# Optimization experiments

Measured on AMD Instinct MI355X. Metric: run time of the kernel, lower is better.

Reference implementation:

```python
import jax, jax.numpy as jnp
import numpy as np

H, HD = 8, 64  # num_heads, head_dim
EPS = 1e-6

def rmsnorm(x, scale):
    return x * jax.lax.rsqrt(jnp.mean(x * x, axis=-1, keepdims=True) + EPS) * scale

def lecun(key, shape):
    fan_in = shape[0]
    return jax.random.normal(key, shape, dtype=jnp.float32) * (fan_in ** -0.5)

def setup_inputs() -> dict:
    key = jax.random.key(0)
    ks = jax.random.split(key, 12)
    B, S, D = 2, 512, 512
    hidden = H * HD            # 512
    ffn = 4 * D                # 2048
    return {
        "inputs": jax.random.normal(ks[0], (B, S, D), dtype=jnp.float32),
        "mask": jnp.zeros((B, S), dtype=jnp.float32),
        "carry": jnp.zeros((B, H, HD, HD), dtype=jnp.float32),
        "ln1": jnp.ones((D,), dtype=jnp.float32),
        "Wq": lecun(ks[1], (D, hidden)),
        "Wk": lecun(ks[2], (D, hidden)),
        "Wv": lecun(ks[3], (D, hidden)),
        "attn_ln": jnp.ones((hidden,), dtype=jnp.float32),
        "Wo": lecun(ks[4], (hidden, D)),
        "bo": jnp.zeros((D,), dtype=jnp.float32),
        "ln2": jnp.ones((D,), dtype=jnp.float32),
        "Wg": lecun(ks[5], (D, ffn)),
        "Wu": lecun(ks[6], (D, ffn)),
        "Wd": lecun(ks[7], (ffn, D)),
    }

def reference(inputs, mask, carry, ln1, Wq, Wk, Wv, attn_ln, Wo, bo, ln2, Wg, Wu, Wd):
    B, S, D = inputs.shape
    skip = inputs
    x = rmsnorm(inputs, ln1)
    # projections + relu feature map
    q = jax.nn.relu((x @ Wq).reshape(B, S, H, HD))
    k = jax.nn.relu((x @ Wk).reshape(B, S, H, HD))
    v = (x @ Wv).reshape(B, S, H, HD)
    # matrix-valued state update: Bmat_t = v_t k_t^T  [B,S,H,HD,HD]
    Bmat = v[..., :, None] * k[..., None, :]
    # decay: identity, zeroed where mask==1 (episode reset)
    m = mask[:, :, None, None, None]
    A = jnp.broadcast_to(jnp.eye(HD, dtype=x.dtype), Bmat.shape) * (1.0 - m)

    def binop(lhs, rhs):
        a_i, b_i = lhs
        a_j, b_j = rhs
        return jnp.matmul(a_i, a_j), jnp.matmul(b_i, a_j) + b_j

    cum_decay, hidden_states = jax.lax.associative_scan(binop, (A, Bmat), axis=1)
    # fold in incoming carry
    states = jnp.matmul(carry[:, None], cum_decay) + hidden_states  # [B,S,H,HD,HD]
    attn = jnp.matmul(states, q[..., None]).squeeze(-1).reshape(B, S, H * HD)
    attn = rmsnorm(attn, attn_ln)
    y = attn @ Wo + bo
    final_carry = states[:, -1]
    # residual + SwiGLU FFN
    x = y + skip
    skip2 = x
    x = rmsnorm(x, ln2)
    x = (jax.nn.silu(x @ Wg) * (x @ Wu)) @ Wd
    return (final_carry, x + skip2)
```

## Files before the change

### kernel.cpp

```cpp
#include <hip/hip_runtime.h>
#include <math.h>

typedef __bf16 bf16x8 __attribute__((ext_vector_type(8)));
typedef float  f32x4  __attribute__((ext_vector_type(4)));

constexpr int B_=2, S_=512, D_=512, H_=8, HD_=64, FFN_=2048, NC_=8;
constexpr float EPS_=1e-6f;

__device__ __forceinline__ __bf16 f2bf(float f){
    union{float f;unsigned u;}x; x.f=f;
    unsigned r=(x.u+0x7fffu+((x.u>>16)&1u))>>16;
    union{unsigned short s;__bf16 b;}y; y.s=(unsigned short)r; return y.b;
}
__device__ __forceinline__ float bf2f(unsigned short s){
    union{unsigned u;float f;}x; x.u=((unsigned)s)<<16; return x.f;
}
__device__ __forceinline__ void bf8_f32(uint4 p, float* o){
    unsigned w[4]={p.x,p.y,p.z,p.w};
#pragma unroll
    for(int i=0;i<4;i++){ o[2*i]=bf2f((unsigned short)(w[i]&0xffffu)); o[2*i+1]=bf2f((unsigned short)(w[i]>>16)); }
}
__device__ __forceinline__ f32x4 MF(bf16x8 a, bf16x8 b, f32x4 c){
    return __builtin_amdgcn_mfma_f32_16x16x32_bf16(a,b,c,0,0,0);
}
#define GLOAD16(g,l) __builtin_amdgcn_global_load_lds((__attribute__((address_space(1))) const void*)(g),(__attribute__((address_space(3))) void*)(l),16,0,0)

__device__ __forceinline__ void rowsq_atomic(float* accb, int row0, int lane, float p[4]){
#pragma unroll
    for(int r=0;r<4;r++){
        float v = p[r];
        v += __shfl_xor(v, 1, 64);
        v += __shfl_xor(v, 2, 64);
        v += __shfl_xor(v, 4, 64);
        v += __shfl_xor(v, 8, 64);
        if((lane&15)==0) atomicAdd(accb + row0 + r, v);
    }
}

__global__ __launch_bounds__(256) void prep_k(const float* __restrict__ Wg,
    const float* __restrict__ Wu, const float* __restrict__ Wd,
    const float* __restrict__ Wq, const float* __restrict__ Wk,
    const float* __restrict__ Wv, const float* __restrict__ Wo,
    __bf16* __restrict__ WT, const float* __restrict__ inputs,
    float* __restrict__ rs1, float* __restrict__ rs2acc, float* __restrict__ rs3acc){
    __shared__ __bf16 s[64][72];
    int t = blockIdx.x, tid = threadIdx.x;
    if(t >= 1024){
        int row = (t-1024)*4 + (tid>>6), lane = tid&63;
        const float4* p = (const float4*)(inputs + (size_t)row*D_) + lane*2;
        float4 a=p[0], b=p[1];
        float ss = a.x*a.x+a.y*a.y+a.z*a.z+a.w*a.w + b.x*b.x+b.y*b.y+b.z*b.z+b.w*b.w;
        for(int off=32; off>0; off>>=1) ss += __shfl_down(ss, off, 64);
        if(lane==0) rs1[row] = rsqrtf(ss/(float)D_ + EPS_);
        float4 z = {0.f,0.f,0.f,0.f};
        if(t==1024) ((float4*)rs2acc)[tid] = z;
        if(t==1025) ((float4*)rs3acc)[tid] = z;
        return;
    }
    const float* src; __bf16* dst; int K,N,lt;
    if      (t<256){ src=Wg; dst=WT;          K=512;  N=2048; lt=t; }
    else if (t<512){ src=Wu; dst=WT+1048576;  K=512;  N=2048; lt=t-256; }
    else if (t<768){ src=Wd; dst=WT+2097152;  K=2048; N=512;  lt=t-512; }
    else if (t<832){ src=Wq; dst=WT+3145728;  K=512;  N=512;  lt=t-768; }
    else if (t<896){ src=Wk; dst=WT+3407872;  K=512;  N=512;  lt=t-832; }
    else if (t<960){ src=Wv; dst=WT+3670016;  K=512;  N=512;  lt=t-896; }
    else           { src=Wo; dst=WT+3932160;  K=512;  N=512;  lt=t-960; }
    int nt64 = N>>6, tk = lt/nt64, tn = lt%nt64;
    {
        int jk = tid>>2, jn0 = (tid&3)*16;
        const float* p = src + (size_t)(tk*64+jk)*N + tn*64 + jn0;
        float4 a0=((const float4*)p)[0], a1=((const float4*)p)[1],
               a2=((const float4*)p)[2], a3=((const float4*)p)[3];
        bf16x8 w0, w1;
        w0[0]=f2bf(a0.x); w0[1]=f2bf(a0.y); w0[2]=f2bf(a0.z); w0[3]=f2bf(a0.w);
        w0[4]=f2bf(a1.x); w0[5]=f2bf(a1.y); w0[6]=f2bf(a1.z); w0[7]=f2bf(a1.w);
        w1[0]=f2bf(a2.x); w1[1]=f2bf(a2.y); w1[2]=f2bf(a2.z); w1[3]=f2bf(a2.w);
        w1[4]=f2bf(a3.x); w1[5]=f2bf(a3.y); w1[6]=f2bf(a3.z); w1[7]=f2bf(a3.w);
        *(bf16x8*)&s[jk][jn0] = w0; *(bf16x8*)&s[jk][jn0+8] = w1;
    }
    __syncthreads();
    {
        int jn = tid&63, jkq = (tid>>6)*16;
        bf16x8 w0, w1;
#pragma unroll
        for(int j=0;j<8;j++){ w0[j]=s[jkq+j][jn]; w1[j]=s[jkq+8+j][jn]; }
        __bf16* q = dst + (size_t)(tn*64+jn)*K + tk*64 + jkq;
        *(bf16x8*)q = w0; *(bf16x8*)(q+8) = w1;
    }
}

__device__ __forceinline__ void stageB1(const __bf16* __restrict__ Bt, int n0, int K, int kk,
                                        __bf16* sB0, __bf16* sB1, int wave, int lane){
    int row = (wave<<4) + (lane>>2), kq = (lane&3)<<3;
    const __bf16* g = Bt + (size_t)(n0+row)*K + kk + kq;
    GLOAD16(g,      sB0 + (wave<<9));
    GLOAD16(g + 32, sB1 + (wave<<9));
}
struct ARf { float4 a0,a1,a2,a3, g0,g1,g2,g3; };
__device__ __forceinline__ ARf loadA_f32(const float* __restrict__ A, const float* __restrict__ g,
                                         int m0, int K, int kk, int tid){
    int row = tid>>2, kq = (tid&3)<<4;
    const float4* p = (const float4*)(A + (size_t)(m0+row)*K + kk + kq);
    const float4* gp = (const float4*)(g + kk + kq);
    ARf o;
    o.a0=p[0]; o.a1=p[1]; o.a2=p[2]; o.a3=p[3];
    o.g0=gp[0]; o.g1=gp[1]; o.g2=gp[2]; o.g3=gp[3];
    return o;
}
__device__ __forceinline__ void writeA_f32(const ARf& o, float r, __bf16* sA0, __bf16* sA1, int tid){
    int row = tid>>2, kq = (tid&3)<<4;
    bf16x8 w0, w1;
    w0[0]=f2bf(o.a0.x*r*o.g0.x); w0[1]=f2bf(o.a0.y*r*o.g0.y);
    w0[2]=f2bf(o.a0.z*r*o.g0.z); w0[3]=f2bf(o.a0.w*r*o.g0.w);
    w0[4]=f2bf(o.a1.x*r*o.g1.x); w0[5]=f2bf(o.a1.y*r*o.g1.y);
    w0[6]=f2bf(o.a1.z*r*o.g1.z); w0[7]=f2bf(o.a1.w*r*o.g1.w);
    w1[0]=f2bf(o.a2.x*r*o.g2.x); w1[1]=f2bf(o.a2.y*r*o.g2.y);
    w1[2]=f2bf(o.a2.z*r*o.g2.z); w1[3]=f2bf(o.a2.w*r*o.g2.w);
    w1[4]=f2bf(o.a3.x*r*o.g3.x); w1[5]=f2bf(o.a3.y*r*o.g3.y);
    w1[6]=f2bf(o.a3.z*r*o.g3.z); w1[7]=f2bf(o.a3.w*r*o.g3.w);
    __bf16* d = (kq<32) ? (sA0 + row*32 + kq) : (sA1 + row*32 + kq-32);
    *(bf16x8*)d = w0; *(bf16x8*)(d+8) = w1;
}
struct ARb { uint4 p0,p1; float4 g0,g1,g2,g3; };
__device__ __forceinline__ ARb loadA_bf16(const __bf16* __restrict__ A, const float* __restrict__ g,
                                          int m0, int K, int kk, int tid){
    int row = tid>>2, kq = (tid&3)<<4;
    const __bf16* p = A + (size_t)(m0+row)*K + kk + kq;
    const float4* gp = (const float4*)(g + kk + kq);
    ARb o;
    o.p0 = *(const uint4*)p; o.p1 = *(const uint4*)(p+8);
    o.g0=gp[0]; o.g1=gp[1]; o.g2=gp[2]; o.g3=gp[3];
    return o;
}
__device__ __forceinline__ void writeA_bf16(const ARb& o, float r, __bf16* sA0, __bf16* sA1, int tid){
    int row = tid>>2, kq = (tid&3)<<4;
    float v[16]; bf8_f32(o.p0, v); bf8_f32(o.p1, v+8);
    float gf[16] = {o.g0.x,o.g0.y,o.g0.z,o.g0.w, o.g1.x,o.g1.y,o.g1.z,o.g1.w,
                    o.g2.x,o.g2.y,o.g2.z,o.g2.w, o.g3.x,o.g3.y,o.g3.z,o.g3.w};
    bf16x8 w0, w1;
#pragma unroll
    for(int j=0;j<8;j++){ w0[j]=f2bf(v[j]*r*gf[j]); w1[j]=f2bf(v[8+j]*r*gf[8+j]); }
    __bf16* d = (kq<32) ? (sA0 + row*32 + kq) : (sA1 + row*32 + kq-32);
    *(bf16x8*)d = w0; *(bf16x8*)(d+8) = w1;
}
__device__ __forceinline__ void mfma_tile(const __bf16* sA0, const __bf16* sA1,
        const __bf16* sB0, const __bf16* sB1, int wave, int lane, f32x4 acc[4]){
    int ar = (((wave<<4)+(lane&15))<<5) + ((lane>>4)<<3);
    bf16x8 a0 = *(const bf16x8*)(sA0+ar);
    bf16x8 a1 = *(const bf16x8*)(sA1+ar);
#pragma unroll
    for(int nt=0;nt<4;nt++){
        int br = (((nt<<4)+(lane&15))<<5) + ((lane>>4)<<3);
        acc[nt] = MF(a0, *(const bf16x8*)(sB0+br), acc[nt]);
        acc[nt] = MF(a1, *(const bf16x8*)(sB1+br), acc[nt]);
    }
}

__global__ __launch_bounds__(256) void gemm_qkv_k(const float* __restrict__ in,
        const float* __restrict__ rs1, const float* __restrict__ ln1,
        const __bf16* __restrict__ Bt, __bf16* __restrict__ Qb,
        __bf16* __restrict__ Kb, __bf16* __restrict__ Vb){
    __shared__ __bf16 sA0[2][2048], sA1[2][2048], sB0[2][2048], sB1[2][2048];
    int tid=threadIdx.x, wave=tid>>6, lane=tid&63;
    int n0 = blockIdx.x*64, m0 = blockIdx.y*64;
    float r = rs1[m0+(tid>>2)];
    f32x4 acc[4] = {};
    {
        ARf a = loadA_f32(in, ln1, m0, 512, 0, tid);
        stageB1(Bt, n0, 512, 0, sB0[0], sB1[0], wave, lane);
        writeA_f32(a, r, sA0[0], sA1[0], tid);
        __syncthreads();
    }
    int cur = 0;
#pragma unroll
    for(int it=0; it<8; ++it){
        int nxt = cur^1;
        ARf a;
        if(it<7){
            a = loadA_f32(in, ln1, m0, 512, (it+1)*64, tid);
            stageB1(Bt, n0, 512, (it+1)*64, sB0[nxt], sB1[nxt], wave, lane);
        }
        mfma_tile(sA0[cur],sA1[cur],sB0[cur],sB1[cur],wave,lane,acc);
        if(it<7) writeA_f32(a, r, sA0[nxt], sA1[nxt], tid);
        __syncthreads();
        cur = nxt;
    }
    int seg = n0>>9, nc = n0&511;
    __bf16* Out = seg==0 ? Qb : (seg==1 ? Kb : Vb);
    bool rl = seg<2;
    __bf16* tile = &sA0[0][0];
    int r0 = (wave<<4) + ((lane>>4)<<2);
#pragma unroll
    for(int nt=0;nt<4;nt++){
        int col = nt*16 + (lane&15);
#pragma unroll
        for(int rr=0;rr<4;rr++){
            float v = acc[nt][rr]; if(rl) v = fmaxf(v,0.f);
            tile[(r0+rr)*64 + col] = f2bf(v);
        }
    }
    __syncthreads();
#pragma unroll
    for(int p=0;p<2;p++){
        int row = (tid>>3) + p*32, c0 = (tid&7)*8;
        *(uint4*)(Out + (size_t)(m0+row)*512 + nc + c0) = *(const uint4*)&tile[row*64 + c0];
    }
}

__global__ __launch_bounds__(256) void scanA_k(const __bf16* __restrict__ Kb,
        const __bf16* __restrict__ Vb, const float* __restrict__ mask,
        __bf16* __restrict__ MS, float* __restrict__ Pws){
    int bid = blockIdx.x;
    int c = bid&7, h = (bid>>3)&7, b = bid>>6;
    __shared__ __bf16 sKT[4096], sVT[4096];
    __shared__ float scv[64], ssp[64];
    int tid = threadIdx.x, wave = tid>>6, lane = tid&63;
    const __bf16* Kg = Kb + (size_t)(b*512 + c*64)*512 + h*64;
    const __bf16* Vg = Vb + (size_t)(b*512 + c*64)*512 + h*64;
    if(tid<64) scv[tid] = 1.f - mask[b*512 + c*64 + tid];
    __syncthreads();
    if(tid==0){
        float sp = 1.f;
        for(int t=63;t>=0;--t){ ssp[t]=sp; sp*=scv[t]; }
        Pws[bid] = sp;
    }
    __syncthreads();
#pragma unroll
    for(int p=0;p<2;p++){
        int t = (tid>>3) + p*32, i0 = (tid&7)*8;
        uint4 kr = *(const uint4*)(Kg + (size_t)t*512 + i0);
        uint4 vr = *(const uint4*)(Vg + (size_t)t*512 + i0);
        const __bf16* kp = (const __bf16*)&kr;
        const unsigned short* vp = (const unsigned short*)&vr;
        float sp = ssp[t];
        __bf16* kh = (t<32) ? sKT : sKT+2048;
        __bf16* vh = (t<32) ? sVT : sVT+2048;
#pragma unroll
        for(int j=0;j<8;j++){
            kh[(i0+j)*32 + (t&31)] = kp[j];
            vh[(i0+j)*32 + (t&31)] = f2bf(bf2f(vp[j])*sp);
        }
    }
    __syncthreads();
    f32x4 am[4] = {};
    mfma_tile(sVT, sVT+2048, sKT, sKT+2048, wave, lane, am);
    __bf16* Mo = MS + (size_t)bid*4096;
    int r0 = (wave<<4) + ((lane>>4)<<2);
#pragma unroll
    for(int nt=0;nt<4;nt++){
        int j = nt*16 + (lane&15);
#pragma unroll
        for(int r=0;r<4;r++) Mo[(size_t)(r0+r)*64 + j] = f2bf(am[nt][r]);
    }
}

__global__ __launch_bounds__(256) void scanC_k(const __bf16* __restrict__ Qb,
        const __bf16* __restrict__ Kb, const __bf16* __restrict__ Vb,
        const float* __restrict__ mask, const __bf16* __restrict__ MS,
        const float* __restrict__ carry, const float* __restrict__ Pws,
        float* __restrict__ carry_out, __bf16* __restrict__ attn,
        float* __restrict__ rs2acc){
    int bid = blockIdx.x;
    int c = bid&7, h = (bid>>3)&7, b = bid>>6;
    int bh = b*H_ + h;
    __shared__ __bf16 sQ[4096], sK[4096], sS[4096], sVT[4096], sW[4096];
    __shared__ float Wtab[64][64];
    __shared__ float scv[64], pp[64];
    int tid = threadIdx.x, wave = tid>>6, lane = tid&63;
    const __bf16* Qg = Qb + (size_t)(b*512 + c*64)*512 + h*64;
    const __bf16* Kg = Kb + (size_t)(b*512 + c*64)*512 + h*64;
    const __bf16* Vg = Vb + (size_t)(b*512 + c*64)*512 + h*64;

    stageB1(Qg, 0, 512, 0, sQ, sQ+2048, wave, lane);
    stageB1(Kg, 0, 512, 0, sK, sK+2048, wave, lane);
    if(tid<64) scv[tid] = 1.f - mask[b*512 + c*64 + tid];
#pragma unroll
    for(int p=0;p<2;p++){
        int u = (tid>>3) + p*32, i0 = (tid&7)*8;
        uint4 vr = *(const uint4*)(Vg + (size_t)u*512 + i0);
        const __bf16* vp = (const __bf16*)&vr;
        __bf16* vh = (u<32) ? sVT : sVT+2048;
#pragma unroll
        for(int j=0;j<8;j++) vh[(i0+j)*32 + (u&31)] = vp[j];
    }
    {
        int i = tid>>2, j0 = (tid&3)*16;
        float s[16];
        const float4* c4 = (const float4*)(carry + (size_t)bh*4096 + i*64 + j0);
        float4 s4[4] = {c4[0],c4[1],c4[2],c4[3]};
        float* sp = (float*)s4;
#pragma unroll
        for(int j=0;j<16;j++) s[j]=sp[j];
        for(int cc=0; cc<c; ++cc){
            float P = Pws[bh*8+cc];
            const __bf16* mp = MS + ((size_t)bh*8+cc)*4096 + i*64 + j0;
            float mv[16]; bf8_f32(*(const uint4*)mp, mv); bf8_f32(*(const uint4*)(mp+8), mv+8);
#pragma unroll
            for(int j=0;j<16;j++) s[j] = s[j]*P + mv[j];
        }
        bf16x8 w0, w1;
#pragma unroll
        for(int j=0;j<8;j++){ w0[j]=f2bf(s[j]); w1[j]=f2bf(s[8+j]); }
        __bf16* d = (j0<32) ? (sS + i*32 + j0) : (sS+2048 + i*32 + j0-32);
        *(bf16x8*)d = w0; *(bf16x8*)(d+8) = w1;
        if(c==7){
            float P = Pws[bh*8+7];
            const __bf16* mp = MS + ((size_t)bh*8+7)*4096 + i*64 + j0;
            float mv[16]; bf8_f32(*(const uint4*)mp, mv); bf8_f32(*(const uint4*)(mp+8), mv+8);
            float4 o4[4];
            float* ov = (float*)o4;
#pragma unroll
            for(int j=0;j<16;j++) ov[j] = s[j]*P + mv[j];
            float4* co = (float4*)(carry_out + (size_t)bh*4096 + i*64 + j0);
            co[0]=o4[0]; co[1]=o4[1]; co[2]=o4[2]; co[3]=o4[3];
        }
    }
    __syncthreads();
    if(tid<64){
        int u = tid; float w = 1.f;
        for(int t=0;t<64;t++){
            if(t>u) w *= scv[t];
            Wtab[u][t] = (t<u) ? 0.f : w;
        }
    }
    if(tid==64){
        float p=1.f;
        for(int t=0;t<64;t++){ p*=scv[t]; pp[t]=p; }
    }
    f32x4 sc[4] = {};
    mfma_tile(sK, sK+2048, sQ, sQ+2048, wave, lane, sc);
    __syncthreads();
    {
        int u0 = (wave<<4) + ((lane>>4)<<2);
#pragma unroll
        for(int nt=0;nt<4;nt++){
            int t = nt*16 + (lane&15);
#pragma unroll
            for(int r=0;r<4;r++){
                int u = u0 + r;
                float v = sc[nt][r] * Wtab[u][t];
                ((u<32)? sW : sW+2048)[t*32 + (u&31)] = f2bf(v);
            }
        }
    }
    __syncthreads();
    f32x4 aI[4] = {}, aX[4] = {};
    mfma_tile(sW, sW+2048, sVT, sVT+2048, wave, lane, aI);
    mfma_tile(sQ, sQ+2048, sS, sS+2048, wave, lane, aX);
    int t0 = (wave<<4) + ((lane>>4)<<2);
    float attv[4][4];
    float psum[4] = {0.f,0.f,0.f,0.f};
#pragma unroll
    for(int nt=0;nt<4;nt++){
#pragma unroll
        for(int r=0;r<4;r++){
            int t = t0 + r;
            float o = aI[nt][r] + aX[nt][r]*pp[t];
            attv[nt][r] = o;
            psum[r] += o*o;
        }
    }
    rowsq_atomic(rs2acc, b*512 + c*64 + t0, lane, psum);
    __syncthreads();
    __bf16* tile = sW;
#pragma unroll
    for(int nt=0;nt<4;nt++){
        int i = nt*16 + (lane&15);
#pragma unroll
        for(int r=0;r<4;r++) tile[(t0+r)*64 + i] = f2bf(attv[nt][r]);
    }
    __syncthreads();
#pragma unroll
    for(int p=0;p<2;p++){
        int row = (tid>>3) + p*32, c0 = (tid&7)*8;
        *(uint4*)(attn + (size_t)(b*512 + c*64 + row)*512 + h*64 + c0) =
            *(const uint4*)&tile[row*64 + c0];
    }
}

__global__ __launch_bounds__(256) void gemm_wo_k(const __bf16* __restrict__ attn,
        const float* __restrict__ rs2acc, const float* __restrict__ aln,
        const __bf16* __restrict__ Bt, const float* __restrict__ bo,
        const float* __restrict__ skip, float* __restrict__ outx,
        __bf16* __restrict__ X1, float* __restrict__ rs3acc){
    __shared__ __bf16 sA0[2][2048], sA1[2][2048], sB0[2][2048], sB1[2][2048];
    int tid=threadIdx.x, wave=tid>>6, lane=tid&63;
    int n0 = blockIdx.x*64, m0 = blockIdx.y*64;
    float r = rsqrtf(rs2acc[m0+(tid>>2)]*(1.f/(float)D_) + EPS_);
    f32x4 acc[4] = {};
    {
        ARb a = loadA_bf16(attn, aln, m0, 512, 0, tid);
        stageB1(Bt, n0, 512, 0, sB0[0], sB1[0], wave, lane);
        writeA_bf16(a, r, sA0[0], sA1[0], tid);
        __syncthreads();
    }
    int cur = 0;
#pragma unroll
    for(int it=0; it<8; ++it){
        int nxt = cur^1;
        ARb a;
        if(it<7){
            a = loadA_bf16(attn, aln, m0, 512, (it+1)*64, tid);
            stageB1(Bt, n0, 512, (it+1)*64, sB0[nxt], sB1[nxt], wave, lane);
        }
        mfma_tile(sA0[cur],sA1[cur],sB0[cur],sB1[cur],wave,lane,acc);
        if(it<7) writeA_bf16(a, r, sA0[nxt], sA1[nxt], tid);
        __syncthreads();
        cur = nxt;
    }
    int r0 = (wave<<4) + ((lane>>4)<<2);
    float psum[4] = {0.f,0.f,0.f,0.f};
    __bf16* tile = &sA0[0][0];
#pragma unroll
    for(int nt=0;nt<4;nt++){
        int col = n0 + nt*16 + (lane&15);
#pragma unroll
        for(int rr=0;rr<4;rr++){
            int row = m0+r0+rr;
            float v = acc[nt][rr] + bo[col] + skip[(size_t)row*512+col];
            outx[(size_t)row*512+col] = v;
            tile[(r0+rr)*64 + nt*16 + (lane&15)] = f2bf(v);
            psum[rr] += v*v;
        }
    }
    rowsq_atomic(rs3acc, m0+r0, lane, psum);
    __syncthreads();
#pragma unroll
    for(int p=0;p<2;p++){
        int row = (tid>>3) + p*32, c0 = (tid&7)*8;
        *(uint4*)(X1 + (size_t)(m0+row)*512 + n0 + c0) = *(const uint4*)&tile[row*64 + c0];
    }
}

__global__ __launch_bounds__(256) void gemm_dual_k(const __bf16* __restrict__ X1,
        const float* __restrict__ rs3acc, const float* __restrict__ ln2,
        const __bf16* __restrict__ Gt, const __bf16* __restrict__ Ut,
        __bf16* __restrict__ Hb){
    __shared__ __bf16 sA0[2][2048], sA1[2][2048];
    __shared__ __bf16 sG0[2][2048], sG1[2][2048], sU0[2][2048], sU1[2][2048];
    int tid=threadIdx.x, wave=tid>>6, lane=tid&63;
    int n0 = blockIdx.x*64, m0 = blockIdx.y*64;
    float r = rsqrtf(rs3acc[m0+(tid>>2)]*(1.f/(float)D_) + EPS_);
    f32x4 ag[4] = {}, au[4] = {};
    {
        ARb a = loadA_bf16(X1, ln2, m0, 512, 0, tid);
        stageB1(Gt, n0, 512, 0, sG0[0], sG1[0], wave, lane);
        stageB1(Ut, n0, 512, 0, sU0[0], sU1[0], wave, lane);
        writeA_bf16(a, r, sA0[0], sA1[0], tid);
        __syncthreads();
    }
    int cur = 0;
#pragma unroll
    for(int it=0; it<8; ++it){
        int nxt = cur^1;
        ARb a;
        if(it<7){
            a = loadA_bf16(X1, ln2, m0, 512, (it+1)*64, tid);
            stageB1(Gt, n0, 512, (it+1)*64, sG0[nxt], sG1[nxt], wave, lane);
            stageB1(Ut, n0, 512, (it+1)*64, sU0[nxt], sU1[nxt], wave, lane);
        }
        {
            int ar = (((wave<<4)+(lane&15))<<5) + ((lane>>4)<<3);
            bf16x8 a0 = *(const bf16x8*)(sA0[cur]+ar);
            bf16x8 a1 = *(const bf16x8*)(sA1[cur]+ar);
#pragma unroll
            for(int nt=0;nt<4;nt++){
                int br = (((nt<<4)+(lane&15))<<5) + ((lane>>4)<<3);
                ag[nt] = MF(a0, *(const bf16x8*)(sG0[cur]+br), ag[nt]);
                ag[nt] = MF(a1, *(const bf16x8*)(sG1[cur]+br), ag[nt]);
                au[nt] = MF(a0, *(const bf16x8*)(sU0[cur]+br), au[nt]);
                au[nt] = MF(a1, *(const bf16x8*)(sU1[cur]+br), au[nt]);
            }
        }
        if(it<7) writeA_bf16(a, r, sA0[nxt], sA1[nxt], tid);
        __syncthreads();
        cur = nxt;
    }
    int r0 = (wave<<4) + ((lane>>4)<<2);
    __bf16* tile = &sA0[0][0];
#pragma unroll
    for(int nt=0;nt<4;nt++){
        int col = nt*16 + (lane&15);
#pragma unroll
        for(int rr=0;rr<4;rr++){
            float gv = ag[nt][rr], uv = au[nt][rr];
            float hv = (gv / (1.f + __expf(-gv))) * uv;
            tile[(r0+rr)*64 + col] = f2bf(hv);
        }
    }
    __syncthreads();
#pragma unroll
    for(int p=0;p<2;p++){
        int row = (tid>>3) + p*32, c0 = (tid&7)*8;
        *(uint4*)(Hb + (size_t)(m0+row)*FFN_ + n0 + c0) = *(const uint4*)&tile[row*64 + c0];
    }
}

__global__ __launch_bounds__(256) void gemm_wd_k(const __bf16* __restrict__ Hb,
        const __bf16* __restrict__ Bt, float* __restrict__ outx){
    __shared__ __bf16 sA0[2][2048], sA1[2][2048], sB0[2][2048], sB1[2][2048];
    int tid=threadIdx.x, wave=tid>>6, lane=tid&63;
    int n0 = blockIdx.x*64, m0 = blockIdx.y*64, ks = blockIdx.z*512;
    f32x4 acc[4] = {};
    int row = (wave<<4) + (lane>>2), kq = (lane&3)<<3;
    {
        stageB1(Bt, n0, FFN_, ks, sB0[0], sB1[0], wave, lane);
        const __bf16* g = Hb + (size_t)(m0+row)*FFN_ + ks + kq;
        GLOAD16(g,      sA0[0] + (wave<<9));
        GLOAD16(g + 32, sA1[0] + (wave<<9));
        __syncthreads();
    }
    int cur = 0;
#pragma unroll
    for(int it=0; it<8; ++it){
        int nxt = cur^1;
        if(it<7){
            int kk = ks + (it+1)*64;
            stageB1(Bt, n0, FFN_, kk, sB0[nxt], sB1[nxt], wave, lane);
            const __bf16* g = Hb + (size_t)(m0+row)*FFN_ + kk + kq;
            GLOAD16(g,      sA0[nxt] + (wave<<9));
            GLOAD16(g + 32, sA1[nxt] + (wave<<9));
        }
        mfma_tile(sA0[cur],sA1[cur],sB0[cur],sB1[cur],wave,lane,acc);
        __syncthreads();
        cur = nxt;
    }
    int r0 = (wave<<4) + ((lane>>4)<<2);
#pragma unroll
    for(int nt=0;nt<4;nt++){
        int col = n0 + nt*16 + (lane&15);
#pragma unroll
        for(int rr=0;rr<4;rr++)
            atomicAdd(&outx[(size_t)(m0+r0+rr)*512 + col], acc[nt][rr]);
    }
}

extern "C" void kernel_launch(void* const* d_in, const int* in_sizes, int n_in,
                              void* d_out, int out_size, void* d_ws, size_t ws_size,
                              hipStream_t stream) {
    const float* inputs  = (const float*)d_in[0];
    const float* mask    = (const float*)d_in[1];
    const float* carry   = (const float*)d_in[2];
    const float* ln1     = (const float*)d_in[3];
    const float* Wq      = (const float*)d_in[4];
    const float* Wk      = (const float*)d_in[5];
    const float* Wv      = (const float*)d_in[6];
    const float* attn_ln = (const float*)d_in[7];
    const float* Wo      = (const float*)d_in[8];
    const float* bo      = (const float*)d_in[9];
    const float* ln2     = (const float*)d_in[10];
    const float* Wg      = (const float*)d_in[11];
    const float* Wu      = (const float*)d_in[12];
    const float* Wd      = (const float*)d_in[13];

    float* out_carry = (float*)d_out;
    float* out_x     = (float*)d_out + 65536;

    __bf16* wb = (__bf16*)d_ws;
    float*  wf = (float*)d_ws;
    __bf16* WgT   = wb;
    __bf16* WuT   = wb + 1048576;
    __bf16* WdT   = wb + 2097152;
    __bf16* WqkvT = wb + 3145728;
    __bf16* WoT   = wb + 3932160;
    __bf16* Qb    = wb + 4194304;
    __bf16* Kb    = wb + 4718592;
    __bf16* Vb    = wb + 5242880;
    __bf16* Hb    = wb + 3145728;
    __bf16* MS    = wb + 5767168;
    float*  Pws   = wf + 3145728;
    float*  rs1   = wf + 3145856;
    float*  rs2a  = wf + 3146880;
    float*  rs3a  = wf + 3147904;

    prep_k<<<dim3(1280), dim3(256), 0, stream>>>(Wg,Wu,Wd,Wq,Wk,Wv,Wo, wb, inputs, rs1, rs2a, rs3a);
    gemm_qkv_k<<<dim3(24,16), dim3(256), 0, stream>>>(inputs, rs1, ln1, WqkvT, Qb, Kb, Vb);
    scanA_k<<<dim3(128), dim3(256), 0, stream>>>(Kb, Vb, mask, MS, Pws);
    scanC_k<<<dim3(128), dim3(256), 0, stream>>>(Qb, Kb, Vb, mask, MS, carry, Pws, out_carry, Qb, rs2a);
    gemm_wo_k<<<dim3(8,16), dim3(256), 0, stream>>>(Qb, rs2a, attn_ln, WoT, bo, inputs, out_x, Vb, rs3a);
    gemm_dual_k<<<dim3(32,16), dim3(256), 0, stream>>>(Vb, rs3a, ln2, WgT, WuT, Hb);
    gemm_wd_k<<<dim3(8,16,4), dim3(256), 0, stream>>>(Hb, WdT, out_x);
}
```

Measured before the change: 162.4 us.

## Preload whole weight K-panels into LDS upfront and double split-K in Wd GEMM

The QKV and Wo GEMMs now load the entire 64x512 B panel (64 KB LDS) into shared memory once, before the main loop, instead of double-buffering it per K-step. The dual Gate/Up GEMM loads half-panels, with a refill at the midpoint. The Wd GEMM doubles split-K to 8 slices of 256, loads all of A and B up front and runs the MFMAs with no per-step barriers. This removes per-iteration B staging and synchronisation, at the cost of much higher LDS use per block (lower occupancy) and twice as many atomic adds in the Wd output.

New measurement: 159.4 us, median of 2. Within noise of the previous version (-1.8%).

```diff
diff --git a/kernel.cpp b/kernel.cpp
--- a/kernel.cpp
+++ b/kernel.cpp
@@ -89,12 +89,12 @@
     }
 }
 
-__device__ __forceinline__ void stageB1(const __bf16* __restrict__ Bt, int n0, int K, int kk,
-                                        __bf16* sB0, __bf16* sB1, int wave, int lane){
+__device__ __forceinline__ void stageTile(const __bf16* __restrict__ Bt, int n0, int K, int kk,
+                                          __bf16* dst, int wave, int lane){
     int row = (wave<<4) + (lane>>2), kq = (lane&3)<<3;
     const __bf16* g = Bt + (size_t)(n0+row)*K + kk + kq;
-    GLOAD16(g,      sB0 + (wave<<9));
-    GLOAD16(g + 32, sB1 + (wave<<9));
+    GLOAD16(g,      dst + (wave<<9));
+    GLOAD16(g + 32, dst + 2048 + (wave<<9));
 }
 struct ARf { float4 a0,a1,a2,a3, g0,g1,g2,g3; };
 __device__ __forceinline__ ARf loadA_f32(const float* __restrict__ A, const float* __restrict__ g,
@@ -107,7 +107,7 @@
     o.g0=gp[0]; o.g1=gp[1]; o.g2=gp[2]; o.g3=gp[3];
     return o;
 }
-__device__ __forceinline__ void writeA_f32(const ARf& o, float r, __bf16* sA0, __bf16* sA1, int tid){
+__device__ __forceinline__ void writeA_f32(const ARf& o, float r, __bf16* sA, int tid){
     int row = tid>>2, kq = (tid&3)<<4;
     bf16x8 w0, w1;
     w0[0]=f2bf(o.a0.x*r*o.g0.x); w0[1]=f2bf(o.a0.y*r*o.g0.y);
@@ -118,7 +118,7 @@
     w1[2]=f2bf(o.a2.z*r*o.g2.z); w1[3]=f2bf(o.a2.w*r*o.g2.w);
     w1[4]=f2bf(o.a3.x*r*o.g3.x); w1[5]=f2bf(o.a3.y*r*o.g3.y);
     w1[6]=f2bf(o.a3.z*r*o.g3.z); w1[7]=f2bf(o.a3.w*r*o.g3.w);
-    __bf16* d = (kq<32) ? (sA0 + row*32 + kq) : (sA1 + row*32 + kq-32);
+    __bf16* d = (kq<32) ? (sA + row*32 + kq) : (sA + 2048 + row*32 + kq-32);
     *(bf16x8*)d = w0; *(bf16x8*)(d+8) = w1;
 }
 struct ARb { uint4 p0,p1; float4 g0,g1,g2,g3; };
@@ -132,7 +132,7 @@
     o.g0=gp[0]; o.g1=gp[1]; o.g2=gp[2]; o.g3=gp[3];
     return o;
 }
-__device__ __forceinline__ void writeA_bf16(const ARb& o, float r, __bf16* sA0, __bf16* sA1, int tid){
+__device__ __forceinline__ void writeA_bf16(const ARb& o, float r, __bf16* sA, int tid){
     int row = tid>>2, kq = (tid&3)<<4;
     float v[16]; bf8_f32(o.p0, v); bf8_f32(o.p1, v+8);
     float gf[16] = {o.g0.x,o.g0.y,o.g0.z,o.g0.w, o.g1.x,o.g1.y,o.g1.z,o.g1.w,
@@ -140,7 +140,7 @@
     bf16x8 w0, w1;
 #pragma unroll
     for(int j=0;j<8;j++){ w0[j]=f2bf(v[j]*r*gf[j]); w1[j]=f2bf(v[8+j]*r*gf[8+j]); }
-    __bf16* d = (kq<32) ? (sA0 + row*32 + kq) : (sA1 + row*32 + kq-32);
+    __bf16* d = (kq<32) ? (sA + row*32 + kq) : (sA + 2048 + row*32 + kq-32);
     *(bf16x8*)d = w0; *(bf16x8*)(d+8) = w1;
 }
 __device__ __forceinline__ void mfma_tile(const __bf16* sA0, const __bf16* sA1,
@@ -160,35 +160,34 @@
         const float* __restrict__ rs1, const float* __restrict__ ln1,
         const __bf16* __restrict__ Bt, __bf16* __restrict__ Qb,
         __bf16* __restrict__ Kb, __bf16* __restrict__ Vb){
-    __shared__ __bf16 sA0[2][2048], sA1[2][2048], sB0[2][2048], sB1[2][2048];
+    __shared__ __bf16 sB[32768];
+    __shared__ __bf16 sA[8192];
     int tid=threadIdx.x, wave=tid>>6, lane=tid&63;
     int n0 = blockIdx.x*64, m0 = blockIdx.y*64;
     float r = rs1[m0+(tid>>2)];
     f32x4 acc[4] = {};
+#pragma unroll
+    for(int t=0;t<8;t++) stageTile(Bt, n0, 512, t*64, sB + t*4096, wave, lane);
     {
         ARf a = loadA_f32(in, ln1, m0, 512, 0, tid);
-        stageB1(Bt, n0, 512, 0, sB0[0], sB1[0], wave, lane);
-        writeA_f32(a, r, sA0[0], sA1[0], tid);
+        writeA_f32(a, r, sA, tid);
+    }
+    __syncthreads();
+    int cur = 0;
+#pragma unroll
+    for(int it=0; it<8; ++it){
+        ARf a;
+        if(it<7) a = loadA_f32(in, ln1, m0, 512, (it+1)*64, tid);
+        const __bf16* bt = sB + it*4096;
+        mfma_tile(sA + cur*4096, sA + cur*4096 + 2048, bt, bt + 2048, wave, lane, acc);
+        if(it<7) writeA_f32(a, r, sA + (cur^1)*4096, tid);
         __syncthreads();
-    }
-    int cur = 0;
-#pragma unroll
-    for(int it=0; it<8; ++it){
-        int nxt = cur^1;
-        ARf a;
-        if(it<7){
-            a = loadA_f32(in, ln1, m0, 512, (it+1)*64, tid);
-            stageB1(Bt, n0, 512, (it+1)*64, sB0[nxt], sB1[nxt], wave, lane);
-        }
-        mfma_tile(sA0[cur],sA1[cur],sB0[cur],sB1[cur],wave,lane,acc);
-        if(it<7) writeA_f32(a, r, sA0[nxt], sA1[nxt], tid);
-        __syncthreads();
-        cur = nxt;
+        cur ^= 1;
     }
     int seg = n0>>9, nc = n0&511;
     __bf16* Out = seg==0 ? Qb : (seg==1 ? Kb : Vb);
     bool rl = seg<2;
-    __bf16* tile = &sA0[0][0];
+    __bf16* tile = sA;
     int r0 = (wave<<4) + ((lane>>4)<<2);
 #pragma unroll
     for(int nt=0;nt<4;nt++){
@@ -271,8 +270,8 @@
     const __bf16* Kg = Kb + (size_t)(b*512 + c*64)*512 + h*64;
     const __bf16* Vg = Vb + (size_t)(b*512 + c*64)*512 + h*64;
 
-    stageB1(Qg, 0, 512, 0, sQ, sQ+2048, wave, lane);
-    stageB1(Kg, 0, 512, 0, sK, sK+2048, wave, lane);
+    stageTile(Qg, 0, 512, 0, sQ, wave, lane);
+    stageTile(Kg, 0, 512, 0, sK, wave, lane);
     if(tid<64) scv[tid] = 1.f - mask[b*512 + c*64 + tid];
 #pragma unroll
     for(int p=0;p<2;p++){
@@ -383,34 +382,33 @@
         const __bf16* __restrict__ Bt, const float* __restrict__ bo,
         const float* __restrict__ skip, float* __restrict__ outx,
         __bf16* __restrict__ X1, float* __restrict__ rs3acc){
-    __shared__ __bf16 sA0[2][2048], sA1[2][2048], sB0[2][2048], sB1[2][2048];
+    __shared__ __bf16 sB[32768];
+    __shared__ __bf16 sA[8192];
     int tid=threadIdx.x, wave=tid>>6, lane=tid&63;
     int n0 = blockIdx.x*64, m0 = blockIdx.y*64;
     float r = rsqrtf(rs2acc[m0+(tid>>2)]*(1.f/(float)D_) + EPS_);
     f32x4 acc[4] = {};
+#pragma unroll
+    for(int t=0;t<8;t++) stageTile(Bt, n0, 512, t*64, sB + t*4096, wave, lane);
     {
         ARb a = loadA_bf16(attn, aln, m0, 512, 0, tid);
-        stageB1(Bt, n0, 512, 0, sB0[0], sB1[0], wave, lane);
-        writeA_bf16(a, r, sA0[0], sA1[0], tid);
+        writeA_bf16(a, r, sA, tid);
+    }
+    __syncthreads();
+    int cur = 0;
+#pragma unroll
+    for(int it=0; it<8; ++it){
+        ARb a;
+        if(it<7) a = loadA_bf16(attn, aln, m0, 512, (it+1)*64, tid);
+        const __bf16* bt = sB + it*4096;
+        mfma_tile(sA + cur*4096, sA + cur*4096 + 2048, bt, bt + 2048, wave, lane, acc);
+        if(it<7) writeA_bf16(a, r, sA + (cur^1)*4096, tid);
         __syncthreads();
-    }
-    int cur = 0;
-#pragma unroll
-    for(int it=0; it<8; ++it){
-        int nxt = cur^1;
-        ARb a;
-        if(it<7){
-            a = loadA_bf16(attn, aln, m0, 512, (it+1)*64, tid);
-            stageB1(Bt, n0, 512, (it+1)*64, sB0[nxt], sB1[nxt], wave, lane);
-        }
-        mfma_tile(sA0[cur],sA1[cur],sB0[cur],sB1[cur],wave,lane,acc);
-        if(it<7) writeA_bf16(a, r, sA0[nxt], sA1[nxt], tid);
-        __syncthreads();
-        cur = nxt;
+        cur ^= 1;
     }
     int r0 = (wave<<4) + ((lane>>4)<<2);
     float psum[4] = {0.f,0.f,0.f,0.f};
-    __bf16* tile = &sA0[0][0];
+    __bf16* tile = sA;
 #pragma unroll
     for(int nt=0;nt<4;nt++){
         int col = n0 + nt*16 + (lane&15);
@@ -436,48 +434,58 @@
         const float* __restrict__ rs3acc, const float* __restrict__ ln2,
         const __bf16* __restrict__ Gt, const __bf16* __restrict__ Ut,
         __bf16* __restrict__ Hb){
-    __shared__ __bf16 sA0[2][2048], sA1[2][2048];
-    __shared__ __bf16 sG0[2][2048], sG1[2][2048], sU0[2][2048], sU1[2][2048];
+    __shared__ __bf16 sG[16384];
+    __shared__ __bf16 sU[16384];
+    __shared__ __bf16 sA[8192];
     int tid=threadIdx.x, wave=tid>>6, lane=tid&63;
     int n0 = blockIdx.x*64, m0 = blockIdx.y*64;
     float r = rsqrtf(rs3acc[m0+(tid>>2)]*(1.f/(float)D_) + EPS_);
     f32x4 ag[4] = {}, au[4] = {};
+#pragma unroll
+    for(int t=0;t<4;t++){
+        stageTile(Gt, n0, 512, t*64, sG + t*4096, wave, lane);
+        stageTile(Ut, n0, 512, t*64, sU + t*4096, wave, lane);
+    }
     {
         ARb a = loadA_bf16(X1, ln2, m0, 512, 0, tid);
-        stageB1(Gt, n0, 512, 0, sG0[0], sG1[0], wave, lane);
-        stageB1(Ut, n0, 512, 0, sU0[0], sU1[0], wave, lane);
-        writeA_bf16(a, r, sA0[0], sA1[0], tid);
-        __syncthreads();
-    }
+        writeA_bf16(a, r, sA, tid);
+    }
+    __syncthreads();
     int cur = 0;
 #pragma unroll
     for(int it=0; it<8; ++it){
-        int nxt = cur^1;
+        if(it==4){
+#pragma unroll
+            for(int t=0;t<4;t++){
+                stageTile(Gt, n0, 512, (4+t)*64, sG + t*4096, wave, lane);
+                stageTile(Ut, n0, 512, (4+t)*64, sU + t*4096, wave, lane);
+            }
+            __syncthreads();
+        }
         ARb a;
-        if(it<7){
-            a = loadA_bf16(X1, ln2, m0, 512, (it+1)*64, tid);
-            stageB1(Gt, n0, 512, (it+1)*64, sG0[nxt], sG1[nxt], wave, lane);
-            stageB1(Ut, n0, 512, (it+1)*64, sU0[nxt], sU1[nxt], wave, lane);
-        }
+        if(it<7) a = loadA_bf16(X1, ln2, m0, 512, (it+1)*64, tid);
         {
+            const __bf16* gt = sG + (it&3)*4096;
+            const __bf16* ut = sU + (it&3)*4096;
             int ar = (((wave<<4)+(lane&15))<<5) + ((lane>>4)<<3);
-            bf16x8 a0 = *(const bf16x8*)(sA0[cur]+ar);
-            bf16x8 a1 = *(const bf16x8*)(sA1[cur]+ar);
+            const __bf16* sAc = sA + cur*4096;
+            bf16x8 a0 = *(const bf16x8*)(sAc+ar);
+            bf16x8 a1 = *(const bf16x8*)(sAc+2048+ar);
 #pragma unroll
             for(int nt=0;nt<4;nt++){
                 int br = (((nt<<4)+(lane&15))<<5) + ((lane>>4)<<3);
-                ag[nt] = MF(a0, *(const bf16x8*)(sG0[cur]+br), ag[nt]);
-                ag[nt] = MF(a1, *(const bf16x8*)(sG1[cur]+br), ag[nt]);
-                au[nt] = MF(a0, *(const bf16x8*)(sU0[cur]+br), au[nt]);
-                au[nt] = MF(a1, *(const bf16x8*)(sU1[cur]+br), au[nt]);
+                ag[nt] = MF(a0, *(const bf16x8*)(gt+br), ag[nt]);
+                ag[nt] = MF(a1, *(const bf16x8*)(gt+2048+br), ag[nt]);
+                au[nt] = MF(a0, *(const bf16x8*)(ut+br), au[nt]);
+                au[nt] = MF(a1, *(const bf16x8*)(ut+2048+br), au[nt]);
             }
         }
-        if(it<7) writeA_bf16(a, r, sA0[nxt], sA1[nxt], tid);
+        if(it<7) writeA_bf16(a, r, sA + (cur^1)*4096, tid);
         __syncthreads();
-        cur = nxt;
+        cur ^= 1;
     }
     int r0 = (wave<<4) + ((lane>>4)<<2);
-    __bf16* tile = &sA0[0][0];
+    __bf16* tile = sA;
 #pragma unroll
     for(int nt=0;nt<4;nt++){
         int col = nt*16 + (lane&15);
@@ -498,32 +506,22 @@
 
 __global__ __launch_bounds__(256) void gemm_wd_k(const __bf16* __restrict__ Hb,
         const __bf16* __restrict__ Bt, float* __restrict__ outx){
-    __shared__ __bf16 sA0[2][2048], sA1[2][2048], sB0[2][2048], sB1[2][2048];
+    __shared__ __bf16 sA[16384];
+    __shared__ __bf16 sB[16384];
     int tid=threadIdx.x, wave=tid>>6, lane=tid&63;
-    int n0 = blockIdx.x*64, m0 = blockIdx.y*64, ks = blockIdx.z*512;
+    int n0 = blockIdx.x*64, m0 = blockIdx.y*64, ks = blockIdx.z*256;
     f32x4 acc[4] = {};
-    int row = (wave<<4) + (lane>>2), kq = (lane&3)<<3;
-    {
-        stageB1(Bt, n0, FFN_, ks, sB0[0], sB1[0], wave, lane);
-        const __bf16* g = Hb + (size_t)(m0+row)*FFN_ + ks + kq;
-        GLOAD16(g,      sA0[0] + (wave<<9));
-        GLOAD16(g + 32, sA1[0] + (wave<<9));
-        __syncthreads();
-    }
-    int cur = 0;
-#pragma unroll
-    for(int it=0; it<8; ++it){
-        int nxt = cur^1;
-        if(it<7){
-            int kk = ks + (it+1)*64;
-            stageB1(Bt, n0, FFN_, kk, sB0[nxt], sB1[nxt], wave, lane);
-            const __bf16* g = Hb + (size_t)(m0+row)*FFN_ + kk + kq;
-            GLOAD16(g,      sA0[nxt] + (wave<<9));
-            GLOAD16(g + 32, sA1[nxt] + (wave<<9));
-        }
-        mfma_tile(sA0[cur],sA1[cur],sB0[cur],sB1[cur],wave,lane,acc);
-        __syncthreads();
-        cur = nxt;
+#pragma unroll
+    for(int t=0;t<4;t++){
+        stageTile(Bt, n0, FFN_, ks + t*64, sB + t*4096, wave, lane);
+        stageTile(Hb, m0, FFN_, ks + t*64, sA + t*4096, wave, lane);
+    }
+    __syncthreads();
+#pragma unroll
+    for(int t=0;t<4;t++){
+        const __bf16* at = sA + t*4096;
+        const __bf16* bt = sB + t*4096;
+        mfma_tile(at, at+2048, bt, bt+2048, wave, lane, acc);
     }
     int r0 = (wave<<4) + ((lane>>4)<<2);
 #pragma unroll
@@ -579,5 +577,5 @@
     scanC_k<<<dim3(128), dim3(256), 0, stream>>>(Qb, Kb, Vb, mask, MS, carry, Pws, out_carry, Qb, rs2a);
     gemm_wo_k<<<dim3(8,16), dim3(256), 0, stream>>>(Qb, rs2a, attn_ln, WoT, bo, inputs, out_x, Vb, rs3a);
     gemm_dual_k<<<dim3(32,16), dim3(256), 0, stream>>>(Vb, rs3a, ln2, WgT, WuT, Hb);
-    gemm_wd_k<<<dim3(8,16,4), dim3(256), 0, stream>>>(Hb, WdT, out_x);
-}
+    gemm_wd_k<<<dim3(8,16,8), dim3(256), 0, stream>>>(Hb, WdT, out_x);
+}
```
